# Kernel optimization log

Hardware: AMD Instinct MI355X
Metric: run time of the kernel (lower is better)

## Reference

```python
import jax, jax.numpy as jnp
import numpy as np

D = 1024
H = 16
DH = D // H

def setup_inputs() -> dict:
    key = jax.random.key(0)
    ks = jax.random.split(key, 9)
    s = 0.02
    return {
        "x": jax.random.normal(ks[0], (2, 2048, D), dtype=jnp.float32),
        "Wq": jax.random.normal(ks[1], (D, D), dtype=jnp.float32) * s,
        "bq": jnp.zeros((D,), dtype=jnp.float32),
        "Wk": jax.random.normal(ks[2], (D, D), dtype=jnp.float32) * s,
        "bk": jnp.zeros((D,), dtype=jnp.float32),
        "Wv": jax.random.normal(ks[3], (D, D), dtype=jnp.float32) * s,
        "bv": jnp.zeros((D,), dtype=jnp.float32),
        "Wo": jax.random.normal(ks[4], (D, D), dtype=jnp.float32) * s,
        "bo": jnp.zeros((D,), dtype=jnp.float32),
    }

def reference(x, Wq, bq, Wk, bk, Wv, bv, Wo, bo):
    B, S, Dm = x.shape
    def proj(W, b):
        # [B,S,D] -> [B,H,S,DH]
        return (x @ W + b).reshape(B, S, H, DH).transpose(0, 2, 1, 3)
    q = proj(Wq, bq)
    k = proj(Wk, bk)
    v = proj(Wv, bv)
    scale = 1.0 / np.sqrt(DH).astype(np.float32)
    raw = jnp.einsum('bhsd,bhtd->bhst', q, k) * scale  # [B,H,S,S]
    w = jax.nn.softmax(raw, axis=-1)
    out = jnp.einsum('bhst,bhtd->bhsd', w, v)          # [B,H,S,DH]
    out = out.transpose(0, 2, 1, 3).reshape(B, S, Dm)
    return out @ Wo + bo
```

## Files before the change

kernel.cpp:

```cpp
#include <hip/hip_runtime.h>
#include <math.h>

constexpr int Dm  = 1024;
constexpr int NH  = 16;
constexpr int SQ  = 2048;
constexpr int NB  = 2;

typedef float f32x4 __attribute__((ext_vector_type(4)));
typedef float f32x16 __attribute__((ext_vector_type(16)));
typedef short bf16x8 __attribute__((ext_vector_type(8)));
typedef __attribute__((address_space(3))) unsigned int lds_u32;
typedef __attribute__((address_space(1))) const unsigned int glb_u32;

__device__ __forceinline__ void gload_lds16(const void* g, void* l) {
    __builtin_amdgcn_global_load_lds((glb_u32*)(uintptr_t)g, (lds_u32*)(uintptr_t)l, 16, 0, 0);
}

__device__ __forceinline__ unsigned short bf_round(float x) {
    unsigned u = __float_as_uint(x);
    unsigned r = u + 0x7fffu + ((u >> 16) & 1u);
    return (unsigned short)(r >> 16);
}

__device__ __forceinline__ float exp2_fast(float x) {
    float r;
    asm("v_exp_f32 %0, %1" : "=v"(r) : "v"(x));
    return r;
}

__device__ __forceinline__ unsigned cvt_pk(float lo, float hi_) {
    unsigned r;
    asm("v_cvt_pk_bf16_f32 %0, %1, %2" : "=v"(r) : "v"(lo), "v"(hi_));
    return r;
}

__device__ __forceinline__ void permlane_swap(unsigned& a, unsigned& b) {
    asm volatile("v_permlane32_swap_b32 %0, %1" : "+v"(a), "+v"(b));
}

__device__ __forceinline__ bf16x8 make_frag(unsigned a, unsigned b, unsigned c, unsigned d) {
    union { unsigned u[4]; bf16x8 v; } uu;
    uu.u[0] = a; uu.u[1] = b; uu.u[2] = c; uu.u[3] = d;
    return uu.v;
}

__global__ __launch_bounds__(256) void prologue(const float* __restrict__ x,
                                                const float* __restrict__ Wq,
                                                const float* __restrict__ Wk,
                                                const float* __restrict__ Wv,
                                                const float* __restrict__ Wo,
                                                unsigned short* __restrict__ xb,
                                                unsigned short* __restrict__ wt) {
    const int z = blockIdx.z;
    const int tid = threadIdx.x;
    if (z == 4) {
        size_t base = ((size_t)blockIdx.y * 16 + blockIdx.x) * 16384;
#pragma unroll
        for (int it = 0; it < 8; ++it) {
            size_t i = base + (size_t)it * 2048 + (size_t)tid * 8;
            float4 a = *(const float4*)&x[i];
            float4 b = *(const float4*)&x[i + 4];
            unsigned short o8[8] __attribute__((aligned(16)));
            o8[0] = bf_round(a.x); o8[1] = bf_round(a.y); o8[2] = bf_round(a.z); o8[3] = bf_round(a.w);
            o8[4] = bf_round(b.x); o8[5] = bf_round(b.y); o8[6] = bf_round(b.z); o8[7] = bf_round(b.w);
            *(uint4*)&xb[i] = *(const uint4*)o8;
        }
        return;
    }
    const float* W = (z == 0) ? Wq : (z == 1) ? Wk : (z == 2) ? Wv : Wo;
    unsigned short* dst = wt + (size_t)z * Dm * Dm;
    __shared__ float T[64][65];
    const int k0 = blockIdx.x * 64, n0 = blockIdx.y * 64;
#pragma unroll
    for (int i = 0; i < 4; ++i) {
        int s = tid + i * 256;
        int kk = s >> 4, c = (s & 15) * 4;
        *(float4*)&T[kk][c] = *(const float4*)&W[(size_t)(k0 + kk) * Dm + n0 + c];
    }
    __syncthreads();
#pragma unroll
    for (int i = 0; i < 2; ++i) {
        int s = tid + i * 256;
        int n = s >> 3, c8 = (s & 7) * 8;
        unsigned short o8[8] __attribute__((aligned(16)));
#pragma unroll
        for (int j = 0; j < 8; ++j) o8[j] = bf_round(T[c8 + j][n]);
        *(uint4*)&dst[(size_t)(n0 + n) * Dm + k0 + c8] = *(const uint4*)o8;
    }
}

__global__ __launch_bounds__(512) void gemm_qkv192(
    const unsigned short* __restrict__ xb,
    const unsigned short* __restrict__ wt,
    const float* __restrict__ bq, const float* __restrict__ bk,
    const float* __restrict__ bv,
    unsigned short* __restrict__ qbuf, unsigned short* __restrict__ kbuf,
    unsigned short* __restrict__ vtbuf)
{
    __shared__ unsigned short Alds[2][256 * 64];
    __shared__ unsigned short Blds[2][192 * 64];

    const int tid = threadIdx.x;
    const int lane = tid & 63, wid = tid >> 6;
    const int wm = wid >> 2, wn = wid & 3;
    const int l15 = lane & 15, lg = lane >> 4;

    const int bid = blockIdx.x;
    const int swz = (bid & 7) * 32 + (bid >> 3);
    const int bx = swz & 15, by = swz >> 4;
    const int m0 = by * 256, n0 = bx * 192;

    const int srow = wid * 8 + (lane >> 3);
    const int scol = ((lane & 7) ^ ((lane >> 3) & 7)) * 8;

    const unsigned short* Abase = xb + (size_t)m0 * Dm;
    const unsigned short* Bbase = wt + (size_t)n0 * Dm;

#define STAGE_TILE(t)                                                              \
    do {                                                                           \
        const unsigned short* As_ = Abase + (t) * 64;                              \
        const unsigned short* Bs_ = Bbase + (t) * 64;                              \
        unsigned short* Ad_ = Alds[(t) & 1];                                       \
        unsigned short* Bd_ = Blds[(t) & 1];                                       \
        _Pragma("unroll")                                                          \
        for (int i_ = 0; i_ < 4; ++i_)                                             \
            gload_lds16(&As_[(size_t)(i_ * 64 + srow) * Dm + scol],                \
                        &Ad_[i_ * 4096 + wid * 512]);                              \
        _Pragma("unroll")                                                          \
        for (int i_ = 0; i_ < 3; ++i_)                                             \
            gload_lds16(&Bs_[(size_t)(i_ * 64 + srow) * Dm + scol],                \
                        &Bd_[i_ * 4096 + wid * 512]);                              \
    } while (0)

    f32x4 acc[8][3];
#pragma unroll
    for (int mr = 0; mr < 8; ++mr)
#pragma unroll
        for (int nr = 0; nr < 3; ++nr) acc[mr][nr] = (f32x4){0.f, 0.f, 0.f, 0.f};

    STAGE_TILE(0);
    asm volatile("s_waitcnt vmcnt(0)" ::: "memory");
    __builtin_amdgcn_s_barrier();

    for (int t = 0; t < Dm / 64; ++t) {
        unsigned short* Ad = Alds[t & 1];
        unsigned short* Bd = Blds[t & 1];
        if (t + 1 < Dm / 64) STAGE_TILE(t + 1);

        bf16x8 a_[4][2], b01[2][2], b2[2];

#define RD_A(qm, fr, ks) \
    (*(const bf16x8*)&Ad[(wm * 128 + (qm) * 64 + (fr) * 16 + l15) * 64 + \
                         ((((ks) * 4 + lg) ^ (l15 & 7)) * 8)])
#define RD_B(fc, ks) \
    (*(const bf16x8*)&Bd[(wn * 48 + (fc) * 16 + l15) * 64 + \
                         ((((ks) * 4 + lg) ^ (l15 & 7)) * 8)])

#pragma unroll
        for (int fr = 0; fr < 4; ++fr) {
            a_[fr][0] = RD_A(0, fr, 0); a_[fr][1] = RD_A(0, fr, 1);
        }
#pragma unroll
        for (int fc = 0; fc < 2; ++fc) {
            b01[fc][0] = RD_B(fc, 0); b01[fc][1] = RD_B(fc, 1);
        }
        __builtin_amdgcn_s_barrier();
        __builtin_amdgcn_s_setprio(1);
#pragma unroll
        for (int fr = 0; fr < 4; ++fr)
#pragma unroll
            for (int fc = 0; fc < 2; ++fc)
#pragma unroll
                for (int ks = 0; ks < 2; ++ks)
                    acc[fr][fc] = __builtin_amdgcn_mfma_f32_16x16x32_bf16(
                        a_[fr][ks], b01[fc][ks], acc[fr][fc], 0, 0, 0);
        __builtin_amdgcn_s_setprio(0);
        __builtin_amdgcn_s_barrier();

        b2[0] = RD_B(2, 0); b2[1] = RD_B(2, 1);
        __builtin_amdgcn_s_barrier();
        __builtin_amdgcn_s_setprio(1);
#pragma unroll
        for (int fr = 0; fr < 4; ++fr)
#pragma unroll
            for (int ks = 0; ks < 2; ++ks)
                acc[fr][2] = __builtin_amdgcn_mfma_f32_16x16x32_bf16(
                    a_[fr][ks], b2[ks], acc[fr][2], 0, 0, 0);
        __builtin_amdgcn_s_setprio(0);
        __builtin_amdgcn_s_barrier();

#pragma unroll
        for (int fr = 0; fr < 4; ++fr) {
            a_[fr][0] = RD_A(1, fr, 0); a_[fr][1] = RD_A(1, fr, 1);
        }
        __builtin_amdgcn_s_barrier();
        __builtin_amdgcn_s_setprio(1);
#pragma unroll
        for (int fr = 0; fr < 4; ++fr)
#pragma unroll
            for (int ks = 0; ks < 2; ++ks)
                acc[4 + fr][2] = __builtin_amdgcn_mfma_f32_16x16x32_bf16(
                    a_[fr][ks], b2[ks], acc[4 + fr][2], 0, 0, 0);
        __builtin_amdgcn_s_setprio(0);
        __builtin_amdgcn_s_barrier();

#pragma unroll
        for (int fc = 0; fc < 2; ++fc) {
            b01[fc][0] = RD_B(fc, 0); b01[fc][1] = RD_B(fc, 1);
        }
        __builtin_amdgcn_s_barrier();
        __builtin_amdgcn_s_setprio(1);
#pragma unroll
        for (int fr = 0; fr < 4; ++fr)
#pragma unroll
            for (int fc = 0; fc < 2; ++fc)
#pragma unroll
                for (int ks = 0; ks < 2; ++ks)
                    acc[4 + fr][fc] = __builtin_amdgcn_mfma_f32_16x16x32_bf16(
                        a_[fr][ks], b01[fc][ks], acc[4 + fr][fc], 0, 0, 0);
        __builtin_amdgcn_s_setprio(0);
        __builtin_amdgcn_s_barrier();

        asm volatile("s_waitcnt vmcnt(0)" ::: "memory");
        __builtin_amdgcn_s_barrier();
#undef RD_A
#undef RD_B
    }

    const float qscale = 0.18033688011f;
#pragma unroll
    for (int mr = 0; mr < 8; ++mr) {
#pragma unroll
        for (int nr = 0; nr < 3; ++nr) {
            const int m = m0 + wm * 128 + mr * 16 + lg * 4;
            const int nglob = n0 + wn * 48 + nr * 16 + l15;
            const int zq = nglob >> 10;
            const int nz = nglob & 1023;
            const float* bias = (zq == 0) ? bq : (zq == 1) ? bk : bv;
            const float bb_ = bias[nz];
            if (zq == 0) {
#pragma unroll
                for (int rr = 0; rr < 4; ++rr)
                    qbuf[(size_t)(m + rr) * Dm + nz] =
                        bf_round((acc[mr][nr][rr] + bb_) * qscale);
            } else if (zq == 1) {
#pragma unroll
                for (int rr = 0; rr < 4; ++rr)
                    kbuf[(size_t)(m + rr) * Dm + nz] = bf_round(acc[mr][nr][rr] + bb_);
            } else {
                const int bbv = m >> 11, s = m & (SQ - 1);
                const int hh = nz >> 6, d = nz & 63;
                unsigned short p4[4] __attribute__((aligned(8)));
#pragma unroll
                for (int rr = 0; rr < 4; ++rr) p4[rr] = bf_round(acc[mr][nr][rr] + bb_);
                *(uint2*)&vtbuf[(((size_t)bbv * NH + hh) * 64 + d) * SQ + s] =
                    *(const uint2*)p4;
            }
        }
    }
#undef STAGE_TILE
}

__global__ __launch_bounds__(256) void gemm_out8(const unsigned short* __restrict__ A,
                                                 const unsigned short* __restrict__ Bt,
                                                 const float* __restrict__ bias,
                                                 float* __restrict__ Cf) {
    __shared__ unsigned short Alds[2][128 * 64];
    __shared__ unsigned short Blds[2][128 * 64];

    const int tid = threadIdx.x;
    const int lane = tid & 63, wid = tid >> 6;
    const int l15 = lane & 15, lg = lane >> 4;
    const int wr = (wid >> 1) * 64, wc = (wid & 1) * 64;
    const int m0 = blockIdx.y * 128, n0 = blockIdx.x * 128;

    const int srow = (tid >> 3) & 31;
    const int scol = ((tid & 7) ^ (srow & 7)) * 8;

    const unsigned short* Abase = A + (size_t)m0 * Dm;
    const unsigned short* Bbase = Bt + (size_t)n0 * Dm;

#define STAGE_TILE(t)                                                              \
    do {                                                                           \
        const unsigned short* As_ = Abase + (t) * 64;                              \
        const unsigned short* Bs_ = Bbase + (t) * 64;                              \
        unsigned short* Ad_ = Alds[(t) & 1];                                       \
        unsigned short* Bd_ = Blds[(t) & 1];                                       \
        _Pragma("unroll")                                                          \
        for (int i_ = 0; i_ < 4; ++i_) {                                           \
            gload_lds16(&As_[(size_t)(i_ * 32 + srow) * Dm + scol],                \
                        &Ad_[i_ * 2048 + wid * 512]);                              \
            gload_lds16(&Bs_[(size_t)(i_ * 32 + srow) * Dm + scol],                \
                        &Bd_[i_ * 2048 + wid * 512]);                              \
        }                                                                          \
    } while (0)

    f32x4 acc[4][4];
#pragma unroll
    for (int r = 0; r < 4; ++r)
#pragma unroll
        for (int c = 0; c < 4; ++c) acc[r][c] = (f32x4){0.f, 0.f, 0.f, 0.f};

    STAGE_TILE(0);
    asm volatile("s_waitcnt vmcnt(0)" ::: "memory");
    __builtin_amdgcn_s_barrier();

    for (int t = 0; t < Dm / 64; ++t) {
        unsigned short* Ad = Alds[t & 1];
        unsigned short* Bd = Blds[t & 1];
        if (t + 1 < Dm / 64) STAGE_TILE(t + 1);

        bf16x8 a_[4][2], b_[2][2];

#define RD_A(fr, ks) \
    (*(const bf16x8*)&Ad[(wr + (fr) * 16 + l15) * 64 + ((((ks) * 4 + lg) ^ (l15 & 7)) * 8)])
#define RD_B(fc, ks) \
    (*(const bf16x8*)&Bd[(wc + (fc) * 16 + l15) * 64 + ((((ks) * 4 + lg) ^ (l15 & 7)) * 8)])

#pragma unroll
        for (int fr = 0; fr < 4; ++fr) {
            a_[fr][0] = RD_A(fr, 0); a_[fr][1] = RD_A(fr, 1);
        }
#pragma unroll
        for (int fc = 0; fc < 2; ++fc) {
            b_[fc][0] = RD_B(fc, 0); b_[fc][1] = RD_B(fc, 1);
        }
        __builtin_amdgcn_s_barrier();
        __builtin_amdgcn_s_setprio(1);
#pragma unroll
        for (int fr = 0; fr < 4; ++fr)
#pragma unroll
            for (int fc = 0; fc < 2; ++fc)
#pragma unroll
                for (int ks = 0; ks < 2; ++ks)
                    acc[fr][fc] = __builtin_amdgcn_mfma_f32_16x16x32_bf16(
                        a_[fr][ks], b_[fc][ks], acc[fr][fc], 0, 0, 0);
        __builtin_amdgcn_s_setprio(0);
        __builtin_amdgcn_s_barrier();

#pragma unroll
        for (int fc = 0; fc < 2; ++fc) {
            b_[fc][0] = RD_B(2 + fc, 0); b_[fc][1] = RD_B(2 + fc, 1);
        }
        __builtin_amdgcn_s_barrier();
        __builtin_amdgcn_s_setprio(1);
#pragma unroll
        for (int fr = 0; fr < 4; ++fr)
#pragma unroll
            for (int fc = 0; fc < 2; ++fc)
#pragma unroll
                for (int ks = 0; ks < 2; ++ks)
                    acc[fr][2 + fc] = __builtin_amdgcn_mfma_f32_16x16x32_bf16(
                        a_[fr][ks], b_[fc][ks], acc[fr][2 + fc], 0, 0, 0);
        __builtin_amdgcn_s_setprio(0);
        __builtin_amdgcn_s_barrier();

        asm volatile("s_waitcnt vmcnt(0)" ::: "memory");
        __builtin_amdgcn_s_barrier();
#undef RD_A
#undef RD_B
    }

#pragma unroll
    for (int r = 0; r < 4; ++r) {
#pragma unroll
        for (int c = 0; c < 4; ++c) {
            const int mBase = m0 + wr + r * 16 + lg * 4;
            const int n = n0 + wc + c * 16 + l15;
            const float bv_ = bias[n];
#pragma unroll
            for (int rr = 0; rr < 4; ++rr)
                Cf[(size_t)(mBase + rr) * Dm + n] = acc[r][c][rr] + bv_;
        }
    }
#undef STAGE_TILE
}

__global__ __launch_bounds__(256) void attn_bf16(const unsigned short* q,
                                                 const unsigned short* __restrict__ k,
                                                 const unsigned short* __restrict__ vt,
                                                 unsigned short* ao) {
    __shared__ unsigned short KVs[2][2][64 * 64];
    const int qt = blockIdx.x, h = blockIdx.y, b = blockIdx.z;
    const int tid = threadIdx.x, lane = tid & 63, wid = tid >> 6;
    const int l31 = lane & 31, hi = lane >> 5;

    const size_t qrow0 = (size_t)b * SQ + qt * 128;
    const unsigned short* qp = q + (qrow0 + wid * 32 + l31) * Dm + h * 64;
    bf16x8 qf[4];
#pragma unroll
    for (int ks = 0; ks < 4; ++ks)
        qf[ks] = *(const bf16x8*)&qp[ks * 16 + hi * 8];

    const unsigned short* kb = k + (size_t)b * SQ * Dm + h * 64;
    const unsigned short* vb = vt + ((size_t)b * NH + h) * 64 * SQ;

    const int row0 = tid >> 3;
    const int s8 = (tid & 7) * 8;
    const int sw8 = (((tid & 7) ^ (row0 & 7))) * 8;
    const int koff0 = row0 * 64 + sw8;
    const int koff1 = (row0 + 32) * 64 + sw8;

    {
        uint4 k0v = *(const uint4*)&kb[(size_t)row0 * Dm + s8];
        uint4 k1v = *(const uint4*)&kb[(size_t)(row0 + 32) * Dm + s8];
        uint4 v0v = *(const uint4*)&vb[(size_t)row0 * SQ + s8];
        uint4 v1v = *(const uint4*)&vb[(size_t)(row0 + 32) * SQ + s8];
        *(uint4*)&KVs[0][0][koff0] = k0v; *(uint4*)&KVs[0][0][koff1] = k1v;
        *(uint4*)&KVs[0][1][koff0] = v0v; *(uint4*)&KVs[0][1][koff1] = v1v;
    }
    __syncthreads();

    float psum = 0.f;
    f32x16 c0, c1;
#pragma unroll
    for (int i = 0; i < 16; ++i) { c0[i] = 0.f; c1[i] = 0.f; }

    int cur = 0;
    for (int t0 = 0; t0 < SQ; t0 += 64) {
        const bool hasNext = (t0 + 64) < SQ;
        uint4 kr0, kr1, vr0, vr1;
        if (hasNext) {
            const unsigned short* kn = kb + (size_t)(t0 + 64) * Dm;
            const unsigned short* vn = vb + (t0 + 64);
            kr0 = *(const uint4*)&kn[(size_t)row0 * Dm + s8];
            kr1 = *(const uint4*)&kn[(size_t)(row0 + 32) * Dm + s8];
            vr0 = *(const uint4*)&vn[(size_t)row0 * SQ + s8];
            vr1 = *(const uint4*)&vn[(size_t)(row0 + 32) * SQ + s8];
        }
        const unsigned short* Kc = KVs[cur][0];
        const unsigned short* Vc = KVs[cur][1];

#pragma unroll
        for (int kblk = 0; kblk < 2; ++kblk) {
            f32x16 p;
#pragma unroll
            for (int i = 0; i < 16; ++i) p[i] = 0.f;
            __builtin_amdgcn_s_setprio(1);
#pragma unroll
            for (int ks = 0; ks < 4; ++ks) {
                int row = kblk * 32 + l31;
                int slot = ((ks * 2 + hi) ^ (l31 & 7)) * 8;
                bf16x8 kf = *(const bf16x8*)&Kc[row * 64 + slot];
                p = __builtin_amdgcn_mfma_f32_32x32x16_bf16(kf, qf[ks], p, 0, 0, 0);
            }
            __builtin_amdgcn_s_setprio(0);

            float e[16];
#pragma unroll
            for (int i = 0; i < 16; ++i) { e[i] = exp2_fast(p[i]); psum += e[i]; }
            unsigned w0 = cvt_pk(e[0], e[1]),   w1 = cvt_pk(e[2], e[3]);
            unsigned w2 = cvt_pk(e[4], e[5]),   w3 = cvt_pk(e[6], e[7]);
            unsigned w4 = cvt_pk(e[8], e[9]),   w5 = cvt_pk(e[10], e[11]);
            unsigned w6 = cvt_pk(e[12], e[13]), w7 = cvt_pk(e[14], e[15]);
            permlane_swap(w0, w2); permlane_swap(w1, w3);
            permlane_swap(w4, w6); permlane_swap(w5, w7);
            bf16x8 pf0 = make_frag(w0, w1, w2, w3);
            bf16x8 pf1 = make_frag(w4, w5, w6, w7);

            int s0 = ((kblk * 4 + hi) ^ (l31 & 7)) * 8;
            int s1 = ((kblk * 4 + 2 + hi) ^ (l31 & 7)) * 8;
            bf16x8 va0 = *(const bf16x8*)&Vc[l31 * 64 + s0];
            bf16x8 va1 = *(const bf16x8*)&Vc[l31 * 64 + s1];
            bf16x8 vb0 = *(const bf16x8*)&Vc[(32 + l31) * 64 + s0];
            bf16x8 vb1 = *(const bf16x8*)&Vc[(32 + l31) * 64 + s1];
            __builtin_amdgcn_s_setprio(1);
            c0 = __builtin_amdgcn_mfma_f32_32x32x16_bf16(va0, pf0, c0, 0, 0, 0);
            c0 = __builtin_amdgcn_mfma_f32_32x32x16_bf16(va1, pf1, c0, 0, 0, 0);
            c1 = __builtin_amdgcn_mfma_f32_32x32x16_bf16(vb0, pf0, c1, 0, 0, 0);
            c1 = __builtin_amdgcn_mfma_f32_32x32x16_bf16(vb1, pf1, c1, 0, 0, 0);
            __builtin_amdgcn_s_setprio(0);
        }

        if (hasNext) {
            unsigned short* Kn = KVs[cur ^ 1][0];
            unsigned short* Vn = KVs[cur ^ 1][1];
            *(uint4*)&Kn[koff0] = kr0; *(uint4*)&Kn[koff1] = kr1;
            *(uint4*)&Vn[koff0] = vr0; *(uint4*)&Vn[koff1] = vr1;
        }
        __syncthreads();
        cur ^= 1;
    }

    float s = psum + __shfl_xor(psum, 32, 64);
    float inv = 1.f / s;

    unsigned short* Olds = (unsigned short*)KVs;
    {
        const int orow = wid * 32 + l31;
#pragma unroll
        for (int db = 0; db < 2; ++db) {
#pragma unroll
            for (int i = 0; i < 8; ++i) {
                float lo  = (db ? c1[2 * i] : c0[2 * i]) * inv;
                float hi_ = (db ? c1[2 * i + 1] : c0[2 * i + 1]) * inv;
                unsigned w = cvt_pk(lo, hi_);
                int d7 = hi * 4 + (i & 1) * 2;
                int slot = db * 4 + (i >> 1);
                int sw = slot ^ (l31 & 7);
                *(unsigned*)&Olds[orow * 64 + sw * 8 + d7] = w;
            }
        }
    }
    __syncthreads();
    {
        int r = tid >> 1, half = tid & 1;
        unsigned short* dst = ao + (qrow0 + r) * Dm + h * 64 + half * 32;
#pragma unroll
        for (int j = 0; j < 4; ++j) {
            int slot = half * 4 + j;
            int sw = slot ^ (r & 7);
            *(uint4*)&dst[j * 8] = *(const uint4*)&Olds[r * 64 + sw * 8];
        }
    }
}

extern "C" void kernel_launch(void* const* d_in, const int* in_sizes, int n_in,
                              void* d_out, int out_size, void* d_ws, size_t ws_size,
                              hipStream_t stream) {
    const float* x  = (const float*)d_in[0];
    const float* Wq = (const float*)d_in[1];
    const float* bq = (const float*)d_in[2];
    const float* Wk = (const float*)d_in[3];
    const float* bk = (const float*)d_in[4];
    const float* Wv = (const float*)d_in[5];
    const float* bv = (const float*)d_in[6];
    const float* Wo = (const float*)d_in[7];
    const float* bo = (const float*)d_in[8];
    float* out = (float*)d_out;

    const size_t M = (size_t)NB * SQ;
    const size_t elems = M * Dm;
    unsigned short* xb    = (unsigned short*)d_ws;
    unsigned short* wtb   = xb + elems;
    unsigned short* qbuf  = wtb + 4ull * Dm * Dm;
    unsigned short* kbuf  = qbuf + elems;
    unsigned short* vtbuf = kbuf + elems;

    dim3 blk(256);
    hipLaunchKernelGGL(prologue, dim3(16, 16, 5), blk, 0, stream,
                       x, Wq, Wk, Wv, Wo, xb, wtb);

    hipLaunchKernelGGL(gemm_qkv192, dim3(256), dim3(512), 0, stream,
                       xb, wtb, bq, bk, bv, qbuf, kbuf, vtbuf);

    hipLaunchKernelGGL(attn_bf16, dim3(SQ / 128, NH, NB), blk, 0, stream,
                       qbuf, kbuf, vtbuf, qbuf);

    hipLaunchKernelGGL(gemm_out8, dim3(Dm / 128, M / 128), blk, 0, stream,
                       qbuf, wtb + 3ull * Dm * Dm, bo, out);
}
```

Baseline: 116.6 us.

## Merge QKV GEMM MFMA phases and double attention KV tile to 128

In the QKV projection GEMM, all three B fragments are now loaded up front and each half of the A tile gets a single MFMA phase. This cuts the per-iteration barrier/setprio phases from four to two and avoids re-reading B fragments from LDS. In the attention kernel, the K/V staging tile grows from 64 to 128 keys, with V stored as 128-wide swizzled rows. That halves the number of __syncthreads and loop iterations per query block. The cost is more registers for prefetch, a shared-memory buffer twice as large (64 KB), and a possible drop in occupancy.

```diff
diff --git a/kernel.cpp b/kernel.cpp
--- a/kernel.cpp
+++ b/kernel.cpp
@@ -147,7 +147,7 @@
         unsigned short* Bd = Blds[t & 1];
         if (t + 1 < Dm / 64) STAGE_TILE(t + 1);
 
-        bf16x8 a_[4][2], b01[2][2], b2[2];
+        bf16x8 a_[4][2], b_[3][2];
 
 #define RD_A(qm, fr, ks) \
     (*(const bf16x8*)&Ad[(wm * 128 + (qm) * 64 + (fr) * 16 + l15) * 64 + \
@@ -161,31 +161,19 @@
             a_[fr][0] = RD_A(0, fr, 0); a_[fr][1] = RD_A(0, fr, 1);
         }
 #pragma unroll
-        for (int fc = 0; fc < 2; ++fc) {
-            b01[fc][0] = RD_B(fc, 0); b01[fc][1] = RD_B(fc, 1);
+        for (int fc = 0; fc < 3; ++fc) {
+            b_[fc][0] = RD_B(fc, 0); b_[fc][1] = RD_B(fc, 1);
         }
         __builtin_amdgcn_s_barrier();
         __builtin_amdgcn_s_setprio(1);
 #pragma unroll
         for (int fr = 0; fr < 4; ++fr)
 #pragma unroll
-            for (int fc = 0; fc < 2; ++fc)
+            for (int fc = 0; fc < 3; ++fc)
 #pragma unroll
                 for (int ks = 0; ks < 2; ++ks)
                     acc[fr][fc] = __builtin_amdgcn_mfma_f32_16x16x32_bf16(
-                        a_[fr][ks], b01[fc][ks], acc[fr][fc], 0, 0, 0);
-        __builtin_amdgcn_s_setprio(0);
-        __builtin_amdgcn_s_barrier();
-
-        b2[0] = RD_B(2, 0); b2[1] = RD_B(2, 1);
-        __builtin_amdgcn_s_barrier();
-        __builtin_amdgcn_s_setprio(1);
-#pragma unroll
-        for (int fr = 0; fr < 4; ++fr)
-#pragma unroll
-            for (int ks = 0; ks < 2; ++ks)
-                acc[fr][2] = __builtin_amdgcn_mfma_f32_16x16x32_bf16(
-                    a_[fr][ks], b2[ks], acc[fr][2], 0, 0, 0);
+                        a_[fr][ks], b_[fc][ks], acc[fr][fc], 0, 0, 0);
         __builtin_amdgcn_s_setprio(0);
         __builtin_amdgcn_s_barrier();
 
@@ -198,26 +186,11 @@
 #pragma unroll
         for (int fr = 0; fr < 4; ++fr)
 #pragma unroll
-            for (int ks = 0; ks < 2; ++ks)
-                acc[4 + fr][2] = __builtin_amdgcn_mfma_f32_16x16x32_bf16(
-                    a_[fr][ks], b2[ks], acc[4 + fr][2], 0, 0, 0);
-        __builtin_amdgcn_s_setprio(0);
-        __builtin_amdgcn_s_barrier();
-
-#pragma unroll
-        for (int fc = 0; fc < 2; ++fc) {
-            b01[fc][0] = RD_B(fc, 0); b01[fc][1] = RD_B(fc, 1);
-        }
-        __builtin_amdgcn_s_barrier();
-        __builtin_amdgcn_s_setprio(1);
-#pragma unroll
-        for (int fr = 0; fr < 4; ++fr)
-#pragma unroll
-            for (int fc = 0; fc < 2; ++fc)
+            for (int fc = 0; fc < 3; ++fc)
 #pragma unroll
                 for (int ks = 0; ks < 2; ++ks)
                     acc[4 + fr][fc] = __builtin_amdgcn_mfma_f32_16x16x32_bf16(
-                        a_[fr][ks], b01[fc][ks], acc[4 + fr][fc], 0, 0, 0);
+                        a_[fr][ks], b_[fc][ks], acc[4 + fr][fc], 0, 0, 0);
         __builtin_amdgcn_s_setprio(0);
         __builtin_amdgcn_s_barrier();
 
@@ -380,7 +353,7 @@
                                                  const unsigned short* __restrict__ k,
                                                  const unsigned short* __restrict__ vt,
                                                  unsigned short* ao) {
-    __shared__ unsigned short KVs[2][2][64 * 64];
+    __shared__ unsigned short KVs[2][2][8192];
     const int qt = blockIdx.x, h = blockIdx.y, b = blockIdx.z;
     const int tid = threadIdx.x, lane = tid & 63, wid = tid >> 6;
     const int l31 = lane & 31, hi = lane >> 5;
@@ -395,20 +368,23 @@
     const unsigned short* kb = k + (size_t)b * SQ * Dm + h * 64;
     const unsigned short* vb = vt + ((size_t)b * NH + h) * 64 * SQ;
 
-    const int row0 = tid >> 3;
-    const int s8 = (tid & 7) * 8;
-    const int sw8 = (((tid & 7) ^ (row0 & 7))) * 8;
-    const int koff0 = row0 * 64 + sw8;
-    const int koff1 = (row0 + 32) * 64 + sw8;
-
-    {
-        uint4 k0v = *(const uint4*)&kb[(size_t)row0 * Dm + s8];
-        uint4 k1v = *(const uint4*)&kb[(size_t)(row0 + 32) * Dm + s8];
-        uint4 v0v = *(const uint4*)&vb[(size_t)row0 * SQ + s8];
-        uint4 v1v = *(const uint4*)&vb[(size_t)(row0 + 32) * SQ + s8];
-        *(uint4*)&KVs[0][0][koff0] = k0v; *(uint4*)&KVs[0][0][koff1] = k1v;
-        *(uint4*)&KVs[0][1][koff0] = v0v; *(uint4*)&KVs[0][1][koff1] = v1v;
-    }
+    const int krow = tid >> 3, ks8 = (tid & 7) * 8;
+    const int ksw = ((tid & 7) ^ (krow & 7)) * 8;
+    const int vrow = tid >> 4, vs8 = (tid & 15) * 8;
+    const int vsw = ((tid & 15) ^ (vrow & 7)) * 8;
+
+#define STAGE_KV(buf, T0)                                                          \
+    do {                                                                           \
+        _Pragma("unroll")                                                          \
+        for (int i_ = 0; i_ < 4; ++i_) {                                           \
+            *(uint4*)&KVs[buf][0][(krow) * 64 + ksw + i_ * 2048] =                 \
+                *(const uint4*)&kb[(size_t)((T0) + krow + 32 * i_) * Dm + ks8];    \
+            *(uint4*)&KVs[buf][1][(vrow) * 128 + vsw + i_ * 2048] =                \
+                *(const uint4*)&vb[(size_t)(vrow + 16 * i_) * SQ + (T0) + vs8];    \
+        }                                                                          \
+    } while (0)
+
+    STAGE_KV(0, 0);
     __syncthreads();
 
     float psum = 0.f;
@@ -417,22 +393,21 @@
     for (int i = 0; i < 16; ++i) { c0[i] = 0.f; c1[i] = 0.f; }
 
     int cur = 0;
-    for (int t0 = 0; t0 < SQ; t0 += 64) {
-        const bool hasNext = (t0 + 64) < SQ;
-        uint4 kr0, kr1, vr0, vr1;
+    for (int t0 = 0; t0 < SQ; t0 += 128) {
+        const bool hasNext = (t0 + 128) < SQ;
+        uint4 kr[4], vr[4];
         if (hasNext) {
-            const unsigned short* kn = kb + (size_t)(t0 + 64) * Dm;
-            const unsigned short* vn = vb + (t0 + 64);
-            kr0 = *(const uint4*)&kn[(size_t)row0 * Dm + s8];
-            kr1 = *(const uint4*)&kn[(size_t)(row0 + 32) * Dm + s8];
-            vr0 = *(const uint4*)&vn[(size_t)row0 * SQ + s8];
-            vr1 = *(const uint4*)&vn[(size_t)(row0 + 32) * SQ + s8];
+#pragma unroll
+            for (int i = 0; i < 4; ++i) {
+                kr[i] = *(const uint4*)&kb[(size_t)(t0 + 128 + krow + 32 * i) * Dm + ks8];
+                vr[i] = *(const uint4*)&vb[(size_t)(vrow + 16 * i) * SQ + t0 + 128 + vs8];
+            }
         }
         const unsigned short* Kc = KVs[cur][0];
         const unsigned short* Vc = KVs[cur][1];
 
 #pragma unroll
-        for (int kblk = 0; kblk < 2; ++kblk) {
+        for (int kblk = 0; kblk < 4; ++kblk) {
             f32x16 p;
 #pragma unroll
             for (int i = 0; i < 16; ++i) p[i] = 0.f;
@@ -460,10 +435,10 @@
 
             int s0 = ((kblk * 4 + hi) ^ (l31 & 7)) * 8;
             int s1 = ((kblk * 4 + 2 + hi) ^ (l31 & 7)) * 8;
-            bf16x8 va0 = *(const bf16x8*)&Vc[l31 * 64 + s0];
-            bf16x8 va1 = *(const bf16x8*)&Vc[l31 * 64 + s1];
-            bf16x8 vb0 = *(const bf16x8*)&Vc[(32 + l31) * 64 + s0];
-            bf16x8 vb1 = *(const bf16x8*)&Vc[(32 + l31) * 64 + s1];
+            bf16x8 va0 = *(const bf16x8*)&Vc[l31 * 128 + s0];
+            bf16x8 va1 = *(const bf16x8*)&Vc[l31 * 128 + s1];
+            bf16x8 vb0 = *(const bf16x8*)&Vc[(32 + l31) * 128 + s0];
+            bf16x8 vb1 = *(const bf16x8*)&Vc[(32 + l31) * 128 + s1];
             __builtin_amdgcn_s_setprio(1);
             c0 = __builtin_amdgcn_mfma_f32_32x32x16_bf16(va0, pf0, c0, 0, 0, 0);
             c0 = __builtin_amdgcn_mfma_f32_32x32x16_bf16(va1, pf1, c0, 0, 0, 0);
@@ -475,8 +450,11 @@
         if (hasNext) {
             unsigned short* Kn = KVs[cur ^ 1][0];
             unsigned short* Vn = KVs[cur ^ 1][1];
-            *(uint4*)&Kn[koff0] = kr0; *(uint4*)&Kn[koff1] = kr1;
-            *(uint4*)&Vn[koff0] = vr0; *(uint4*)&Vn[koff1] = vr1;
+#pragma unroll
+            for (int i = 0; i < 4; ++i) {
+                *(uint4*)&Kn[krow * 64 + ksw + i * 2048] = kr[i];
+                *(uint4*)&Vn[vrow * 128 + vsw + i * 2048] = vr[i];
+            }
         }
         __syncthreads();
         cur ^= 1;
@@ -513,6 +491,7 @@
             *(uint4*)&dst[j * 8] = *(const uint4*)&Olds[r * 64 + sw * 8];
         }
     }
+#undef STAGE_KV
 }
 
 extern "C" void kernel_launch(void* const* d_in, const int* in_sizes, int n_in,
```

After: 137.0 us. 17.5% more time.
